# Kernel tuning notes

Measured on AMD Instinct MI355X. Metric: run time of the kernel, lower is better.

The kernel has to match this reference:

```python
import jax, jax.numpy as jnp
import numpy as np

N_NODES = 100000
N_EDGES = 50000
D = 128        # node feature dim
NNZ = 1600000  # number of (node, hyperedge) incidence pairs


def setup_inputs() -> dict:
    key = jax.random.key(0)
    k1, k2, k3, k4, k5 = jax.random.split(key, 5)
    y = jax.random.normal(k1, (N_NODES * D,), dtype=jnp.float32)
    node_idx = jax.random.randint(k2, (NNZ,), 0, N_NODES, dtype=jnp.int32)
    edge_idx = jax.random.randint(k3, (NNZ,), 0, N_EDGES, dtype=jnp.int32)
    incidence = jnp.stack([node_idx, edge_idx])  # [2, NNZ]
    scale = jnp.float32(1.0 / np.sqrt(D))
    W1 = jax.random.normal(k4, (D, D), dtype=jnp.float32) * scale
    W2 = jax.random.normal(k5, (D, D), dtype=jnp.float32) * scale
    b1 = jnp.zeros((D,), dtype=jnp.float32)
    b2 = jnp.zeros((D,), dtype=jnp.float32)
    return {"t": jnp.float32(0.0), "y": y, "incidence": incidence,
            "W1": W1, "b1": b1, "W2": W2, "b2": b2}


def reference(t, y, incidence, W1, b1, W2, b2):
    # reshape flat SDE state to (n, d) -- the wrapper's core job
    X = y.reshape(N_NODES, D)
    n_idx = incidence[0]
    e_idx = incidence[1]
    ones = jnp.ones((NNZ,), dtype=X.dtype)

    # node -> hyperedge: linear map, gather by node, mean-aggregate per edge
    msg = X @ W1 + b1                                   # [n, d]
    edge_sum = jax.ops.segment_sum(msg[n_idx], e_idx, num_segments=N_EDGES)
    edge_deg = jax.ops.segment_sum(ones, e_idx, num_segments=N_EDGES)
    edge_feat = edge_sum / jnp.maximum(edge_deg, 1.0)[:, None]  # [e, d]

    # hyperedge -> node: linear map, gather by edge, mean-aggregate per node
    out_msg = edge_feat @ W2 + b2                       # [e, d]
    node_sum = jax.ops.segment_sum(out_msg[e_idx], n_idx, num_segments=N_NODES)
    node_deg = jax.ops.segment_sum(ones, n_idx, num_segments=N_NODES)
    x_new = node_sum / jnp.maximum(node_deg, 1.0)[:, None]      # [n, d]

    # activation + flatten back to 1D drift
    return jax.nn.relu(x_new).reshape(-1)
```

## Files before the change

### kernel.cpp

```cpp
#include <hip/hip_runtime.h>

#define NN_NODES 100000
#define NN_EDGES 50000
#define DD 128
#define NNZP 1600000
#define NT_SEG (NN_EDGES + NN_NODES)
#define TOTP (2 * NNZP)
#define BKT_SHIFT 9
#define NBKT ((NT_SEG + 511) / 512)
#define TILE 8192
#define NBIN ((TOTP + TILE - 1) / TILE)
#define CVTBLK 1024
#define SMAX 18432
#define CAP 20480

typedef unsigned int uint;
typedef unsigned short ushort;
typedef __attribute__((ext_vector_type(8))) short bf16x8;
typedef __attribute__((ext_vector_type(4))) float f32x4;

__device__ __forceinline__ float bf_lo(uint u) {
  union { uint i; float f; } c; c.i = u << 16; return c.f;
}
__device__ __forceinline__ float bf_hi(uint u) {
  union { uint i; float f; } c; c.i = u & 0xffff0000u; return c.f;
}
__device__ __forceinline__ ushort f2bf(float f) {
  union { float f; uint i; } c; c.f = f;
  uint r = c.i + 0x7fffu + ((c.i >> 16) & 1u);
  return (ushort)(r >> 16);
}

__device__ __forceinline__ void block_excl_scan_512(const int* __restrict__ arr,
                                                    int* __restrict__ out,
                                                    int* __restrict__ wsum) {
  int t = threadIdx.x;
  int v = arr[t];
  int lane = t & 63, wid = t >> 6;
  int s = v;
  #pragma unroll
  for (int o = 1; o < 64; o <<= 1) {
    int u = __shfl_up(s, o, 64);
    if (lane >= o) s += u;
  }
  if (lane == 63) wsum[wid] = s;
  __syncthreads();
  int add = 0;
  for (int w = 0; w < wid; ++w) add += wsum[w];
  out[t] = s + add - v;
}

__global__ __launch_bounds__(256) void k_wc(const float* __restrict__ W1,
                                            const float* __restrict__ W2,
                                            const float* __restrict__ b1,
                                            const float* __restrict__ b2,
                                            ushort* __restrict__ Wct,
                                            float* __restrict__ bc) {
  __shared__ float sW2[DD * DD];
  __shared__ float sW1[8 * DD];
  const int b = blockIdx.x;
  for (int i = threadIdx.x; i < DD * 32; i += 256)
    reinterpret_cast<float4*>(sW2)[i] = reinterpret_cast<const float4*>(W2)[i];
  for (int i = threadIdx.x; i < 8 * 32; i += 256)
    reinterpret_cast<float4*>(sW1)[i] = reinterpret_cast<const float4*>(W1 + b * 8 * DD)[i];
  __syncthreads();
  const int lr = threadIdx.x >> 5;
  const int cg = threadIdx.x & 31;
  float s0 = 0.f, s1 = 0.f, s2 = 0.f, s3 = 0.f;
  for (int k = 0; k < DD; ++k) {
    float a = sW1[lr * DD + k];
    float4 w = reinterpret_cast<const float4*>(sW2)[k * 32 + cg];
    s0 += a * w.x; s1 += a * w.y; s2 += a * w.z; s3 += a * w.w;
  }
  const int grow = b * 8 + lr;
  const int c0 = cg * 4;
  Wct[(size_t)(c0 + 0) * DD + grow] = f2bf(s0);
  Wct[(size_t)(c0 + 1) * DD + grow] = f2bf(s1);
  Wct[(size_t)(c0 + 2) * DD + grow] = f2bf(s2);
  Wct[(size_t)(c0 + 3) * DD + grow] = f2bf(s3);
  if (b == 0 && threadIdx.x < DD) {
    float s = b2[threadIdx.x];
    for (int k = 0; k < DD; ++k) s += b1[k] * sW2[k * DD + threadIdx.x];
    bc[threadIdx.x] = s;
  }
}

__global__ __launch_bounds__(512) void k_bin(const int* __restrict__ ninc,
                                             const int* __restrict__ einc,
                                             int* __restrict__ bktcur,
                                             int* __restrict__ bval,
                                             ushort* __restrict__ blow,
                                             const float* __restrict__ X,
                                             ushort* __restrict__ Xb) {
  const int b = blockIdx.x;
  if (b >= NBIN) {
    const int stride = CVTBLK * 512;
    for (int i = (b - NBIN) * 512 + threadIdx.x; i < NN_NODES * DD / 4; i += stride) {
      float4 v = reinterpret_cast<const float4*>(X)[i];
      ushort4 o;
      o.x = f2bf(v.x); o.y = f2bf(v.y); o.z = f2bf(v.z); o.w = f2bf(v.w);
      reinterpret_cast<ushort4*>(Xb)[i] = o;
    }
    return;
  }
  __shared__ int sval[TILE];
  __shared__ ushort slow[TILE], sbkt[TILE];
  __shared__ int bhist[512], bexcl[512], bcur[512], brun[512], wsum[8];
  const int t = threadIdx.x;
  const int i0 = b * TILE;
  const int V = min(TILE, TOTP - i0);
  int pseg[16], pval[16];
  bhist[t] = 0;
  __syncthreads();
  #pragma unroll
  for (int j = 0; j < 16; ++j) {
    int e = t + j * 512;
    if (e < V) {
      int i = i0 + e;
      int seg, val;
      if (i < NNZP) { seg = einc[i]; val = ninc[i]; }
      else          { seg = NN_EDGES + ninc[i - NNZP]; val = einc[i - NNZP]; }
      pseg[j] = seg; pval[j] = val;
      atomicAdd(&bhist[seg >> BKT_SHIFT], 1);
    }
  }
  __syncthreads();
  block_excl_scan_512(bhist, bexcl, wsum);
  __syncthreads();
  if (t < NBKT && bhist[t] > 0)
    brun[t] = t * CAP + atomicAdd(&bktcur[t], bhist[t]);
  bcur[t] = bexcl[t];
  __syncthreads();
  #pragma unroll
  for (int j = 0; j < 16; ++j) {
    int e = t + j * 512;
    if (e < V) {
      int bk = pseg[j] >> BKT_SHIFT;
      int slot = atomicAdd(&bcur[bk], 1);
      sval[slot] = pval[j];
      slow[slot] = (ushort)(pseg[j] & 511);
      sbkt[slot] = (ushort)bk;
    }
  }
  __syncthreads();
  for (int e = t; e < V; e += 512) {
    int bk = sbkt[e];
    int gpos = brun[bk] + (e - bexcl[bk]);
    if (gpos < (bk + 1) * CAP) {
      bval[gpos] = sval[e];
      blow[gpos] = slow[e];
    }
  }
}

__global__ void k_bscan(const int* __restrict__ bktcnt, int* __restrict__ bktbase,
                        int* __restrict__ offs) {
  __shared__ int arr[512], out[512], wsum[8];
  int t = threadIdx.x;
  arr[t] = (t < NBKT) ? min(bktcnt[t], CAP) : 0;
  __syncthreads();
  block_excl_scan_512(arr, out, wsum);
  __syncthreads();
  bktbase[t] = out[t];
  if (t == 0) offs[NT_SEG] = TOTP;
}

__global__ __launch_bounds__(512) void k_place(const int* __restrict__ bktbase,
                                               const int* __restrict__ bktcnt,
                                               const int* __restrict__ bval,
                                               const ushort* __restrict__ blow,
                                               int* __restrict__ offs,
                                               int* __restrict__ list) {
  __shared__ int shist[512], sexcl[512], scur[512], wsum[8];
  __shared__ int stage[SMAX];
  const int b = blockIdx.x;
  const int t = threadIdx.x;
  const int base = bktbase[b];
  const int sb = b * CAP;
  const int s = min(bktcnt[b], CAP);
  shist[t] = 0;
  __syncthreads();
  for (int e = t; e < s; e += 512) atomicAdd(&shist[blow[sb + e]], 1);
  __syncthreads();
  block_excl_scan_512(shist, sexcl, wsum);
  __syncthreads();
  int seg = (b << BKT_SHIFT) + t;
  if (seg < NT_SEG) offs[seg] = base + sexcl[t];
  scur[t] = sexcl[t];
  __syncthreads();
  if (s <= SMAX) {
    for (int e = t; e < s; e += 512) {
      int slot = atomicAdd(&scur[blow[sb + e]], 1);
      stage[slot] = bval[sb + e];
    }
    __syncthreads();
    for (int e = t; e < s; e += 512) list[base + e] = stage[e];
  } else {
    for (int e = t; e < s; e += 512) {
      int r = atomicAdd(&scur[blow[sb + e]], 1);
      list[base + r] = bval[sb + e];
    }
  }
}

#define ACC8(V) do { \
    acc[0] += bf_lo(V.x); acc[1] += bf_hi(V.x); \
    acc[2] += bf_lo(V.y); acc[3] += bf_hi(V.y); \
    acc[4] += bf_lo(V.z); acc[5] += bf_hi(V.z); \
    acc[6] += bf_lo(V.w); acc[7] += bf_hi(V.w); } while (0)

template<int MODE>
__global__ __launch_bounds__(256) void k_agg(const ushort* __restrict__ src,
                                             void* __restrict__ dstv,
                                             const float* __restrict__ bias,
                                             const int* __restrict__ offs,
                                             const int* __restrict__ list,
                                             int nseg, int segbase) {
  int g = (int)((blockIdx.x * blockDim.x + threadIdx.x) >> 4);
  int t = threadIdx.x & 15;
  if (g >= nseg) return;
  int b0 = offs[segbase + g];
  int deg = offs[segbase + g + 1] - b0;
  float acc[8];
  #pragma unroll
  for (int j = 0; j < 8; ++j) acc[j] = 0.f;
  const int* lp = list + b0;
  int ida[8];
  #pragma unroll
  for (int j = 0; j < 8; ++j) ida[j] = lp[j];
  int chunk = 0;
  while (chunk + 8 <= deg) {
    uint4 vb[8];
    #pragma unroll
    for (int j = 0; j < 8; ++j)
      vb[j] = reinterpret_cast<const uint4*>(src + (size_t)ida[j] * DD)[t];
    int idb[8];
    #pragma unroll
    for (int j = 0; j < 8; ++j) idb[j] = lp[chunk + 8 + j];
    #pragma unroll
    for (int j = 0; j < 8; ++j) ACC8(vb[j]);
    #pragma unroll
    for (int j = 0; j < 8; ++j) ida[j] = idb[j];
    chunk += 8;
  }
  #pragma unroll
  for (int j = 0; j < 8; ++j) {
    if (chunk + j < deg) {
      uint4 v = reinterpret_cast<const uint4*>(src + (size_t)ida[j] * DD)[t];
      ACC8(v);
    }
  }
  float inv = 1.0f / fmaxf((float)deg, 1.0f);
  if (MODE == 0) {
    ushort* dst = (ushort*)dstv;
    uint4 o;
    o.x = (uint)f2bf(acc[0] * inv) | ((uint)f2bf(acc[1] * inv) << 16);
    o.y = (uint)f2bf(acc[2] * inv) | ((uint)f2bf(acc[3] * inv) << 16);
    o.z = (uint)f2bf(acc[4] * inv) | ((uint)f2bf(acc[5] * inv) << 16);
    o.w = (uint)f2bf(acc[6] * inv) | ((uint)f2bf(acc[7] * inv) << 16);
    reinterpret_cast<uint4*>(dst + (size_t)g * DD)[t] = o;
  } else {
    float flag = (deg > 0) ? 1.f : 0.f;
    float4 bb0 = reinterpret_cast<const float4*>(bias)[2 * t];
    float4 bb1 = reinterpret_cast<const float4*>(bias)[2 * t + 1];
    float4 o0, o1;
    o0.x = fmaxf(acc[0] * inv + bb0.x * flag, 0.f);
    o0.y = fmaxf(acc[1] * inv + bb0.y * flag, 0.f);
    o0.z = fmaxf(acc[2] * inv + bb0.z * flag, 0.f);
    o0.w = fmaxf(acc[3] * inv + bb0.w * flag, 0.f);
    o1.x = fmaxf(acc[4] * inv + bb1.x * flag, 0.f);
    o1.y = fmaxf(acc[5] * inv + bb1.y * flag, 0.f);
    o1.z = fmaxf(acc[6] * inv + bb1.z * flag, 0.f);
    o1.w = fmaxf(acc[7] * inv + bb1.w * flag, 0.f);
    float* orow = (float*)dstv + (size_t)g * DD;
    reinterpret_cast<float4*>(orow)[2 * t] = o0;
    reinterpret_cast<float4*>(orow)[2 * t + 1] = o1;
  }
}

template<int RELU, int CBF16, int BIASED>
__global__ __launch_bounds__(256) void k_gemm_mfma(
    const ushort* __restrict__ A, void* __restrict__ Cv,
    const ushort* __restrict__ Wt, const float* __restrict__ bias,
    const int* __restrict__ segoff, int M) {
  __shared__ ushort sA[DD * DD];
  __shared__ ushort sW[DD * DD];
  const int tid = threadIdx.x;
  const int R = blockIdx.x * DD;
  const int rows = min(DD, M - R);
  for (int i = tid; i < DD * 16; i += 256) {
    int r = i >> 4, c8 = i & 15;
    uint4 v = reinterpret_cast<const uint4*>(Wt + (size_t)r * DD)[c8];
    int bo = (c8 * 16) ^ ((r & 7) << 4);
    *reinterpret_cast<uint4*>(reinterpret_cast<char*>(sW) + r * 256 + bo) = v;
  }
  for (int i = tid; i < DD * 16; i += 256) {
    int r = i >> 4, c8 = i & 15;
    uint4 v = make_uint4(0u, 0u, 0u, 0u);
    if (r < rows) v = reinterpret_cast<const uint4*>(A + (size_t)(R + r) * DD)[c8];
    int bo = (c8 * 16) ^ ((r & 7) << 4);
    *reinterpret_cast<uint4*>(reinterpret_cast<char*>(sA) + r * 256 + bo) = v;
  }
  __syncthreads();
  const int wid = tid >> 6;
  const int l = tid & 63;
  const int lr = l & 15;
  const int lg = l >> 4;
  const int wrow = wid * 32;
  f32x4 acc[2][8];
  #pragma unroll
  for (int a = 0; a < 2; ++a)
    #pragma unroll
    for (int b = 0; b < 8; ++b) acc[a][b] = (f32x4){0.f, 0.f, 0.f, 0.f};
  const char* cA = reinterpret_cast<const char*>(sA);
  const char* cW = reinterpret_cast<const char*>(sW);
  #pragma unroll
  for (int k0 = 0; k0 < 4; ++k0) {
    int kb = k0 * 64 + lg * 16;
    int r0 = wrow + lr, r1 = wrow + 16 + lr;
    bf16x8 a0 = *reinterpret_cast<const bf16x8*>(cA + r0 * 256 + (kb ^ ((r0 & 7) << 4)));
    bf16x8 a1 = *reinterpret_cast<const bf16x8*>(cA + r1 * 256 + (kb ^ ((r1 & 7) << 4)));
    bf16x8 bfr[8];
    #pragma unroll
    for (int ct = 0; ct < 8; ++ct) {
      int c = ct * 16 + lr;
      bfr[ct] = *reinterpret_cast<const bf16x8*>(cW + c * 256 + (kb ^ ((c & 7) << 4)));
    }
    #pragma unroll
    for (int ct = 0; ct < 8; ++ct) {
      acc[0][ct] = __builtin_amdgcn_mfma_f32_16x16x32_bf16(a0, bfr[ct], acc[0][ct], 0, 0, 0);
      acc[1][ct] = __builtin_amdgcn_mfma_f32_16x16x32_bf16(a1, bfr[ct], acc[1][ct], 0, 0, 0);
    }
  }
  float bcol[8];
  if (BIASED) {
    #pragma unroll
    for (int ct = 0; ct < 8; ++ct) bcol[ct] = bias[ct * 16 + lr];
  }
  #pragma unroll
  for (int rt = 0; rt < 2; ++rt) {
    #pragma unroll
    for (int j = 0; j < 4; ++j) {
      int r = wrow + rt * 16 + lg * 4 + j;
      if (r < rows) {
        int gr = R + r;
        float flag = 0.f;
        if (BIASED) flag = (segoff[gr + 1] > segoff[gr]) ? 1.f : 0.f;
        #pragma unroll
        for (int ct = 0; ct < 8; ++ct) {
          float v = acc[rt][ct][j];
          if (BIASED) v += bcol[ct] * flag;
          if (RELU) v = fmaxf(v, 0.f);
          if (CBF16)
            reinterpret_cast<ushort*>(Cv)[(size_t)gr * DD + ct * 16 + lr] = f2bf(v);
          else
            reinterpret_cast<float*>(Cv)[(size_t)gr * DD + ct * 16 + lr] = v;
        }
      }
    }
  }
}

extern "C" void kernel_launch(void* const* d_in, const int* in_sizes, int n_in,
                              void* d_out, int out_size, void* d_ws, size_t ws_size,
                              hipStream_t stream) {
  const float* X   = (const float*)d_in[1];
  const int*   inc = (const int*)d_in[2];
  const float* W1  = (const float*)d_in[3];
  const float* b1  = (const float*)d_in[4];
  const float* W2  = (const float*)d_in[5];
  const float* b2  = (const float*)d_in[6];
  float* out = (float*)d_out;
  const int* ninc = inc;
  const int* einc = inc + NNZP;

  char* wsp = (char*)d_ws;
  int* bval    = (int*)wsp;    wsp += (size_t)NBKT * CAP * sizeof(int);
  ushort* blow = (ushort*)wsp; wsp += (size_t)NBKT * CAP * sizeof(ushort);
  ushort* Xb   = (ushort*)wsp; wsp += (size_t)NN_NODES * DD * sizeof(ushort);
  int* offs    = (int*)wsp;    wsp += (size_t)(NT_SEG + 1) * sizeof(int);
  int* list    = (int*)wsp;    wsp += (size_t)TOTP * sizeof(int);
  int* bktcur  = (int*)wsp;    wsp += 512 * sizeof(int);
  int* bktbase = (int*)wsp;    wsp += 512 * sizeof(int);
  ushort* Wct  = (ushort*)wsp; wsp += (size_t)DD * DD * sizeof(ushort);
  float* bc    = (float*)wsp;  wsp += DD * sizeof(float);
  ushort* bufE = (ushort*)bval;

  hipMemsetAsync(bktcur, 0, 512 * sizeof(int), stream);

  k_wc<<<16, 256, 0, stream>>>(W1, W2, b1, b2, Wct, bc);
  k_bin<<<NBIN + CVTBLK, 512, 0, stream>>>(ninc, einc, bktcur, bval, blow, X, Xb);
  k_bscan<<<1, 512, 0, stream>>>(bktcur, bktbase, offs);
  k_place<<<NBKT, 512, 0, stream>>>(bktbase, bktcur, bval, blow, offs, list);

  k_agg<0><<<(NN_EDGES * 16 + 255) / 256, 256, 0, stream>>>(Xb, bufE, nullptr, offs, list, NN_EDGES, 0);
  k_gemm_mfma<0, 1, 0><<<(NN_EDGES + DD - 1) / DD, 256, 0, stream>>>(bufE, bufE, Wct, nullptr, nullptr, NN_EDGES);
  k_agg<1><<<(NN_NODES * 16 + 255) / 256, 256, 0, stream>>>(bufE, out, bc, offs, list, NN_NODES, NN_EDGES);
}
```

Before: 198.5 us.

## Fuse weight precompute and bucket scan into binning kernels, pack bucket payloads

Folds the W1·W2 weight-combination kernel into extra blocks of the binning kernel and removes the separate bucket-scan kernel by having each placement block compute its own base prefix over bucket counts. Bucket entries are packed into one int (9-bit low segment id, 20-bit value), dropping the separate ushort array. The tail of the aggregation loop is restructured to issue all remaining gathers before accumulating. This cuts two launches and some memory traffic, at the cost of redundant prefix work in every placement block and W2 read from global memory instead of shared memory.

```diff
diff --git a/kernel.cpp b/kernel.cpp
--- a/kernel.cpp
+++ b/kernel.cpp
@@ -13,6 +13,7 @@
 #define CVTBLK 1024
 #define SMAX 18432
 #define CAP 20480
+#define VMASK 0xFFFFF
 
 typedef unsigned int uint;
 typedef unsigned short ushort;
@@ -50,52 +51,56 @@
   out[t] = s + add - v;
 }
 
-__global__ __launch_bounds__(256) void k_wc(const float* __restrict__ W1,
-                                            const float* __restrict__ W2,
-                                            const float* __restrict__ b1,
-                                            const float* __restrict__ b2,
-                                            ushort* __restrict__ Wct,
-                                            float* __restrict__ bc) {
-  __shared__ float sW2[DD * DD];
-  __shared__ float sW1[8 * DD];
-  const int b = blockIdx.x;
-  for (int i = threadIdx.x; i < DD * 32; i += 256)
-    reinterpret_cast<float4*>(sW2)[i] = reinterpret_cast<const float4*>(W2)[i];
-  for (int i = threadIdx.x; i < 8 * 32; i += 256)
-    reinterpret_cast<float4*>(sW1)[i] = reinterpret_cast<const float4*>(W1 + b * 8 * DD)[i];
-  __syncthreads();
-  const int lr = threadIdx.x >> 5;
-  const int cg = threadIdx.x & 31;
-  float s0 = 0.f, s1 = 0.f, s2 = 0.f, s3 = 0.f;
-  for (int k = 0; k < DD; ++k) {
-    float a = sW1[lr * DD + k];
-    float4 w = reinterpret_cast<const float4*>(sW2)[k * 32 + cg];
-    s0 += a * w.x; s1 += a * w.y; s2 += a * w.z; s3 += a * w.w;
-  }
-  const int grow = b * 8 + lr;
-  const int c0 = cg * 4;
-  Wct[(size_t)(c0 + 0) * DD + grow] = f2bf(s0);
-  Wct[(size_t)(c0 + 1) * DD + grow] = f2bf(s1);
-  Wct[(size_t)(c0 + 2) * DD + grow] = f2bf(s2);
-  Wct[(size_t)(c0 + 3) * DD + grow] = f2bf(s3);
-  if (b == 0 && threadIdx.x < DD) {
-    float s = b2[threadIdx.x];
-    for (int k = 0; k < DD; ++k) s += b1[k] * sW2[k * DD + threadIdx.x];
-    bc[threadIdx.x] = s;
-  }
-}
-
 __global__ __launch_bounds__(512) void k_bin(const int* __restrict__ ninc,
                                              const int* __restrict__ einc,
                                              int* __restrict__ bktcur,
-                                             int* __restrict__ bval,
-                                             ushort* __restrict__ blow,
+                                             int* __restrict__ pbuf,
                                              const float* __restrict__ X,
-                                             ushort* __restrict__ Xb) {
+                                             ushort* __restrict__ Xb,
+                                             const float* __restrict__ W1,
+                                             const float* __restrict__ W2,
+                                             const float* __restrict__ b1,
+                                             const float* __restrict__ b2,
+                                             ushort* __restrict__ Wct,
+                                             float* __restrict__ bc) {
+  __shared__ int spack[TILE];
+  __shared__ ushort sbkt[TILE];
+  __shared__ int bhist[512], bexcl[512], bcur[512], brun[512], wsum[8];
   const int b = blockIdx.x;
+  const int t = threadIdx.x;
+  if (b >= NBIN + CVTBLK) {
+    const int bb = b - NBIN - CVTBLK;
+    float* sW1 = (float*)spack;
+    for (int i = t; i < 8 * 32; i += 512)
+      reinterpret_cast<float4*>(sW1)[i] = reinterpret_cast<const float4*>(W1 + bb * 8 * DD)[i];
+    __syncthreads();
+    if (t < 256) {
+      const int lr = t >> 5;
+      const int cg = t & 31;
+      float s0 = 0.f, s1 = 0.f, s2 = 0.f, s3 = 0.f;
+      for (int j = 0; j < DD; ++j) {
+        float a = sW1[lr * DD + j];
+        float4 w = reinterpret_cast<const float4*>(W2)[j * 32 + cg];
+        s0 += a * w.x; s1 += a * w.y; s2 += a * w.z; s3 += a * w.w;
+      }
+      const int grow = bb * 8 + lr;
+      const int c0 = cg * 4;
+      Wct[(size_t)(c0 + 0) * DD + grow] = f2bf(s0);
+      Wct[(size_t)(c0 + 1) * DD + grow] = f2bf(s1);
+      Wct[(size_t)(c0 + 2) * DD + grow] = f2bf(s2);
+      Wct[(size_t)(c0 + 3) * DD + grow] = f2bf(s3);
+    }
+    if (bb == 0 && t >= 256 && t < 256 + DD) {
+      int c = t - 256;
+      float s = b2[c];
+      for (int j = 0; j < DD; ++j) s += b1[j] * W2[(size_t)j * DD + c];
+      bc[c] = s;
+    }
+    return;
+  }
   if (b >= NBIN) {
     const int stride = CVTBLK * 512;
-    for (int i = (b - NBIN) * 512 + threadIdx.x; i < NN_NODES * DD / 4; i += stride) {
+    for (int i = (b - NBIN) * 512 + t; i < NN_NODES * DD / 4; i += stride) {
       float4 v = reinterpret_cast<const float4*>(X)[i];
       ushort4 o;
       o.x = f2bf(v.x); o.y = f2bf(v.y); o.z = f2bf(v.z); o.w = f2bf(v.w);
@@ -103,10 +108,6 @@
     }
     return;
   }
-  __shared__ int sval[TILE];
-  __shared__ ushort slow[TILE], sbkt[TILE];
-  __shared__ int bhist[512], bexcl[512], bcur[512], brun[512], wsum[8];
-  const int t = threadIdx.x;
   const int i0 = b * TILE;
   const int V = min(TILE, TOTP - i0);
   int pseg[16], pval[16];
@@ -137,8 +138,7 @@
     if (e < V) {
       int bk = pseg[j] >> BKT_SHIFT;
       int slot = atomicAdd(&bcur[bk], 1);
-      sval[slot] = pval[j];
-      slow[slot] = (ushort)(pseg[j] & 511);
+      spack[slot] = ((pseg[j] & 511) << 20) | pval[j];
       sbkt[slot] = (ushort)bk;
     }
   }
@@ -146,59 +146,53 @@
   for (int e = t; e < V; e += 512) {
     int bk = sbkt[e];
     int gpos = brun[bk] + (e - bexcl[bk]);
-    if (gpos < (bk + 1) * CAP) {
-      bval[gpos] = sval[e];
-      blow[gpos] = slow[e];
-    }
-  }
-}
-
-__global__ void k_bscan(const int* __restrict__ bktcnt, int* __restrict__ bktbase,
-                        int* __restrict__ offs) {
-  __shared__ int arr[512], out[512], wsum[8];
-  int t = threadIdx.x;
-  arr[t] = (t < NBKT) ? min(bktcnt[t], CAP) : 0;
-  __syncthreads();
-  block_excl_scan_512(arr, out, wsum);
-  __syncthreads();
-  bktbase[t] = out[t];
-  if (t == 0) offs[NT_SEG] = TOTP;
-}
-
-__global__ __launch_bounds__(512) void k_place(const int* __restrict__ bktbase,
-                                               const int* __restrict__ bktcnt,
-                                               const int* __restrict__ bval,
-                                               const ushort* __restrict__ blow,
+    if (gpos < (bk + 1) * CAP)
+      pbuf[gpos] = spack[e];
+  }
+}
+
+__global__ __launch_bounds__(512) void k_place(const int* __restrict__ bktcnt,
+                                               const int* __restrict__ pbuf,
                                                int* __restrict__ offs,
                                                int* __restrict__ list) {
-  __shared__ int shist[512], sexcl[512], scur[512], wsum[8];
+  __shared__ int shist[512], sexcl[512], scur[512], wsum[8], red[8];
   __shared__ int stage[SMAX];
   const int b = blockIdx.x;
   const int t = threadIdx.x;
-  const int base = bktbase[b];
+  int part = 0;
+  for (int i = t; i < b; i += 512) part += min(bktcnt[i], CAP);
+  #pragma unroll
+  for (int o = 1; o < 64; o <<= 1) part += __shfl_xor(part, o, 64);
+  if ((t & 63) == 0) red[t >> 6] = part;
+  shist[t] = 0;
+  __syncthreads();
+  int base = 0;
+  #pragma unroll
+  for (int w = 0; w < 8; ++w) base += red[w];
   const int sb = b * CAP;
   const int s = min(bktcnt[b], CAP);
-  shist[t] = 0;
-  __syncthreads();
-  for (int e = t; e < s; e += 512) atomicAdd(&shist[blow[sb + e]], 1);
+  for (int e = t; e < s; e += 512) atomicAdd(&shist[pbuf[sb + e] >> 20], 1);
   __syncthreads();
   block_excl_scan_512(shist, sexcl, wsum);
   __syncthreads();
   int seg = (b << BKT_SHIFT) + t;
   if (seg < NT_SEG) offs[seg] = base + sexcl[t];
+  if (b == 0 && t == 0) offs[NT_SEG] = TOTP;
   scur[t] = sexcl[t];
   __syncthreads();
   if (s <= SMAX) {
     for (int e = t; e < s; e += 512) {
-      int slot = atomicAdd(&scur[blow[sb + e]], 1);
-      stage[slot] = bval[sb + e];
+      int p = pbuf[sb + e];
+      int slot = atomicAdd(&scur[p >> 20], 1);
+      stage[slot] = p & VMASK;
     }
     __syncthreads();
     for (int e = t; e < s; e += 512) list[base + e] = stage[e];
   } else {
     for (int e = t; e < s; e += 512) {
-      int r = atomicAdd(&scur[blow[sb + e]], 1);
-      list[base + r] = bval[sb + e];
+      int p = pbuf[sb + e];
+      int r = atomicAdd(&scur[p >> 20], 1);
+      list[base + r] = p & VMASK;
     }
   }
 }
@@ -243,12 +237,17 @@
     for (int j = 0; j < 8; ++j) ida[j] = idb[j];
     chunk += 8;
   }
-  #pragma unroll
-  for (int j = 0; j < 8; ++j) {
-    if (chunk + j < deg) {
-      uint4 v = reinterpret_cast<const uint4*>(src + (size_t)ida[j] * DD)[t];
-      ACC8(v);
-    }
+  if (chunk < deg) {
+    uint4 vb[8];
+    #pragma unroll
+    for (int j = 0; j < 8; ++j) {
+      uint4 v = make_uint4(0u, 0u, 0u, 0u);
+      if (chunk + j < deg)
+        v = reinterpret_cast<const uint4*>(src + (size_t)ida[j] * DD)[t];
+      vb[j] = v;
+    }
+    #pragma unroll
+    for (int j = 0; j < 8; ++j) ACC8(vb[j]);
   }
   float inv = 1.0f / fmaxf((float)deg, 1.0f);
   if (MODE == 0) {
@@ -278,11 +277,9 @@
   }
 }
 
-template<int RELU, int CBF16, int BIASED>
 __global__ __launch_bounds__(256) void k_gemm_mfma(
-    const ushort* __restrict__ A, void* __restrict__ Cv,
-    const ushort* __restrict__ Wt, const float* __restrict__ bias,
-    const int* __restrict__ segoff, int M) {
+    const ushort* __restrict__ A, ushort* __restrict__ C,
+    const ushort* __restrict__ Wt, int M) {
   __shared__ ushort sA[DD * DD];
   __shared__ ushort sW[DD * DD];
   const int tid = threadIdx.x;
@@ -332,11 +329,6 @@
       acc[1][ct] = __builtin_amdgcn_mfma_f32_16x16x32_bf16(a1, bfr[ct], acc[1][ct], 0, 0, 0);
     }
   }
-  float bcol[8];
-  if (BIASED) {
-    #pragma unroll
-    for (int ct = 0; ct < 8; ++ct) bcol[ct] = bias[ct * 16 + lr];
-  }
   #pragma unroll
   for (int rt = 0; rt < 2; ++rt) {
     #pragma unroll
@@ -344,18 +336,9 @@
       int r = wrow + rt * 16 + lg * 4 + j;
       if (r < rows) {
         int gr = R + r;
-        float flag = 0.f;
-        if (BIASED) flag = (segoff[gr + 1] > segoff[gr]) ? 1.f : 0.f;
         #pragma unroll
-        for (int ct = 0; ct < 8; ++ct) {
-          float v = acc[rt][ct][j];
-          if (BIASED) v += bcol[ct] * flag;
-          if (RELU) v = fmaxf(v, 0.f);
-          if (CBF16)
-            reinterpret_cast<ushort*>(Cv)[(size_t)gr * DD + ct * 16 + lr] = f2bf(v);
-          else
-            reinterpret_cast<float*>(Cv)[(size_t)gr * DD + ct * 16 + lr] = v;
-        }
+        for (int ct = 0; ct < 8; ++ct)
+          C[(size_t)gr * DD + ct * 16 + lr] = f2bf(acc[rt][ct][j]);
       }
     }
   }
@@ -375,25 +358,22 @@
   const int* einc = inc + NNZP;
 
   char* wsp = (char*)d_ws;
-  int* bval    = (int*)wsp;    wsp += (size_t)NBKT * CAP * sizeof(int);
-  ushort* blow = (ushort*)wsp; wsp += (size_t)NBKT * CAP * sizeof(ushort);
+  int* pbuf    = (int*)wsp;    wsp += (size_t)NBKT * CAP * sizeof(int);
   ushort* Xb   = (ushort*)wsp; wsp += (size_t)NN_NODES * DD * sizeof(ushort);
   int* offs    = (int*)wsp;    wsp += (size_t)(NT_SEG + 1) * sizeof(int);
   int* list    = (int*)wsp;    wsp += (size_t)TOTP * sizeof(int);
   int* bktcur  = (int*)wsp;    wsp += 512 * sizeof(int);
-  int* bktbase = (int*)wsp;    wsp += 512 * sizeof(int);
   ushort* Wct  = (ushort*)wsp; wsp += (size_t)DD * DD * sizeof(ushort);
   float* bc    = (float*)wsp;  wsp += DD * sizeof(float);
-  ushort* bufE = (ushort*)bval;
+  ushort* bufE = (ushort*)pbuf;
 
   hipMemsetAsync(bktcur, 0, 512 * sizeof(int), stream);
 
-  k_wc<<<16, 256, 0, stream>>>(W1, W2, b1, b2, Wct, bc);
-  k_bin<<<NBIN + CVTBLK, 512, 0, stream>>>(ninc, einc, bktcur, bval, blow, X, Xb);
-  k_bscan<<<1, 512, 0, stream>>>(bktcur, bktbase, offs);
-  k_place<<<NBKT, 512, 0, stream>>>(bktbase, bktcur, bval, blow, offs, list);
+  k_bin<<<NBIN + CVTBLK + 16, 512, 0, stream>>>(ninc, einc, bktcur, pbuf,
+                                                X, Xb, W1, W2, b1, b2, Wct, bc);
+  k_place<<<NBKT, 512, 0, stream>>>(bktcur, pbuf, offs, list);
 
   k_agg<0><<<(NN_EDGES * 16 + 255) / 256, 256, 0, stream>>>(Xb, bufE, nullptr, offs, list, NN_EDGES, 0);
-  k_gemm_mfma<0, 1, 0><<<(NN_EDGES + DD - 1) / DD, 256, 0, stream>>>(bufE, bufE, Wct, nullptr, nullptr, NN_EDGES);
+  k_gemm_mfma<<<(NN_EDGES + DD - 1) / DD, 256, 0, stream>>>(bufE, bufE, Wct, NN_EDGES);
   k_agg<1><<<(NN_NODES * 16 + 255) / 256, 256, 0, stream>>>(bufE, out, bc, offs, list, NN_NODES, NN_EDGES);
 }
```

Measured after the change: 173.8 us, median of 2. 1.14x faster.
